# Kernel optimization log

Hardware: AMD Instinct MI355X
Metric: run time of the kernel (lower is better)

The kernel has to match this reference:

```python
import jax, jax.numpy as jnp
import numpy as np
from jax import lax

# config constants (match init_kwargs)
SEQ_LEN = 512
PRED_LEN = 96
ENC_IN = 64
D_MODEL = 128
E_LAYERS = 2
GRAPH_SCALE = 16
GRAPH_RANK = 8
TCN_KERNEL = 3
TCN_DILATION = 2
BATCH = 16


def setup_inputs() -> dict:
    key = jax.random.key(0)
    ks = jax.random.split(key, 12)
    s = 0.02
    inp = {
        "x_enc": jax.random.normal(ks[0], (BATCH, SEQ_LEN, ENC_IN), jnp.float32),
        "x_mark_enc": jnp.zeros((BATCH, SEQ_LEN, 4), jnp.float32),
        "x_dec": jnp.zeros((BATCH, PRED_LEN, ENC_IN), jnp.float32),
        "x_mark_dec": jnp.zeros((BATCH, PRED_LEN, 4), jnp.float32),
        # value embedding (scalar -> d_model)
        "w_emb": jax.random.normal(ks[1], (1, D_MODEL), jnp.float32) * s,
        "b_emb": jnp.zeros((D_MODEL,), jnp.float32),
        # stacked dilated causal conv layers [L, K, Cin, Cout]
        "conv_w": jax.random.normal(ks[2], (E_LAYERS, TCN_KERNEL, D_MODEL, D_MODEL), jnp.float32) * s,
        "conv_b": jnp.zeros((E_LAYERS, D_MODEL), jnp.float32),
        # low-rank graph generator projections
        "gg_w1": jax.random.normal(ks[3], (D_MODEL, GRAPH_RANK), jnp.float32) * s,
        "gg_b1": jnp.zeros((GRAPH_RANK,), jnp.float32),
        "gg_w2": jax.random.normal(ks[4], (D_MODEL, GRAPH_RANK), jnp.float32) * s,
        "gg_b2": jnp.zeros((GRAPH_RANK,), jnp.float32),
        # head: Linear(d_model * num_tokens, pred_len)
        "head_w": jax.random.normal(ks[5], (D_MODEL * SEQ_LEN, PRED_LEN), jnp.float32) * s,
        "head_b": jnp.zeros((PRED_LEN,), jnp.float32),
    }
    return inp


def _tcn(x_enc, w_emb, b_emb, conv_w, conv_b):
    # x_enc: [B, L, N] -> channel-independent per-variable encoding -> [B, N, L, D]
    B, L, N = x_enc.shape
    h = x_enc.transpose(0, 2, 1).reshape(B * N, L, 1) @ w_emb + b_emb  # [B*N, L, D]
    for i in range(conv_w.shape[0]):
        dil = TCN_DILATION ** i
        pad = (TCN_KERNEL - 1) * dil
        hp = jnp.pad(h, ((0, 0), (pad, 0), (0, 0)))  # causal left pad
        y = lax.conv_general_dilated(
            hp, conv_w[i], window_strides=(1,), padding="VALID",
            rhs_dilation=(dil,), dimension_numbers=("NWC", "WIO", "NWC"),
        ) + conv_b[i]
        h = jax.nn.gelu(y) + h  # residual
    return h.reshape(B, N, L, -1)


def _forward(x_enc, w_emb, b_emb, conv_w, conv_b, gg_w1, gg_b1, gg_w2, gg_b2, head_w, head_b):
    h_time = _tcn(x_enc, w_emb, b_emb, conv_w, conv_b)  # [B, N, L, D]
    B, N, L, D = h_time.shape
    S = L // GRAPH_SCALE  # number of segments (L divisible by scale)
    h_seg = h_time.reshape(B, N, S, GRAPH_SCALE, D)
    z = h_seg.mean(axis=3)  # [B, N, S, D] segment summaries
    # low-rank graph generation for all segments at once
    e1 = z @ gg_w1 + gg_b1  # [B, N, S, r]
    e2 = z @ gg_w2 + gg_b2
    scores = jnp.einsum("bnsr,bmsr->bsnm", e1, e2) / jnp.asarray(np.sqrt(GRAPH_RANK), z.dtype)
    adj = jax.nn.softmax(scores, axis=-1)  # [B, S, N, N] row-stochastic
    # adjacency temporal-smoothness regularizer: sum_s mean|adj_s - adj_{s-1}|
    reg = jnp.sum(jnp.mean(jnp.abs(adj[:, 1:] - adj[:, :-1]), axis=(0, 2, 3)))
    # graph-weighted feature mixing per segment
    h_mix = jnp.einsum("bsnm,bmscd->bnscd", adj, h_seg).reshape(B, N, L, D)
    # head over flattened (token, dim)
    out = h_mix.reshape(B, N, L * D) @ head_w + head_b  # [B, N, pred_len]
    return out.transpose(0, 2, 1), reg  # [B, pred_len, N]


def reference(x_enc, x_mark_enc, x_dec, x_mark_dec, w_emb, b_emb, conv_w, conv_b,
              gg_w1, gg_b1, gg_w2, gg_b2, head_w, head_b):
    # x_mark_enc / x_dec / x_mark_dec are unused by forecast path (faithful to source)
    return _forward(x_enc, w_emb, b_emb, conv_w, conv_b, gg_w1, gg_b1, gg_w2, gg_b2, head_w, head_b)
```

## Files before the change

kernel.cpp:

```cpp
#include <hip/hip_runtime.h>
#include <hip/hip_bf16.h>


#define BATCH 16
#define SEQ 512
#define NVAR 64
#define DM 128
#define SEG 32
#define SCL 16
#define RNK 8
#define PRED 96
#define BN (BATCH * NVAR)
#define ROWLEN (SEQ * DM)

typedef unsigned short ushort_t;
typedef __attribute__((ext_vector_type(8))) short short8;
typedef __attribute__((ext_vector_type(4))) float f32x4;

__device__ inline float bf2f(ushort_t u) {
    union { unsigned int i; float f; } x;
    x.i = ((unsigned int)u) << 16;
    return x.f;
}
__device__ inline ushort_t f2bf(float f) {
    union { float f; unsigned int i; } u;
    u.f = f;
    unsigned int x = u.i;
    return (ushort_t)((x + 0x7fffu + ((x >> 16) & 1u)) >> 16);
}
__device__ inline unsigned int pkbf(float a, float b) {
    __hip_bfloat162 h = __float22bfloat162_rn(make_float2(a, b));
    union { __hip_bfloat162 h2; unsigned int u; } c;
    c.h2 = h;
    return c.u;
}
__device__ inline float blo(unsigned int u) {
    union { unsigned int i; float f; } x;
    x.i = u << 16;
    return x.f;
}
__device__ inline float bhi(unsigned int u) {
    union { unsigned int i; float f; } x;
    x.i = u & 0xFFFF0000u;
    return x.f;
}
__device__ inline float gelu_fast(float x) {
    float t = 0.7978845608028654f * x * (1.0f + 0.044715f * x * x);
    float e = __expf(-2.0f * t);
    return x * __builtin_amdgcn_rcpf(1.0f + e);
}

__global__ __launch_bounds__(128) void wt_prep(
    const float* __restrict__ conv_w, const float* __restrict__ w_emb,
    const float* __restrict__ b_emb, const float* __restrict__ conv_b,
    ushort_t* __restrict__ WTf, float* __restrict__ Acoef,
    float* __restrict__ Bias3, float* __restrict__ regacc) {
    if (blockIdx.x == 0 && blockIdx.y == 0 && threadIdx.x == 0) regacc[0] = 0.f;
    if (blockIdx.x < 3) {
        int tap = blockIdx.x;
        int ci = blockIdx.y;
        int co = threadIdx.x;
        int kt = ci >> 5, quad = (ci >> 3) & 3, j = ci & 7;
        int ng = co >> 4, col = co & 15;
        int lane = quad * 16 + col;
        WTf[((((size_t)tap * 4 + kt) * 8 + ng) * 64 + lane) * 8 + j] =
            f2bf(conv_w[(size_t)(3 + tap) * 16384 + (size_t)ci * 128 + co]);
    } else if (blockIdx.y == 0) {
        int co = threadIdx.x;
        float a0 = 0.f, a1 = 0.f, a2 = 0.f, c0 = 0.f, c1 = 0.f, c2 = 0.f;
        for (int ci = 0; ci < 128; ++ci) {
            float we = w_emb[ci], be = b_emb[ci];
            float w0 = conv_w[((size_t)(0 * 128 + ci)) * 128 + co];
            float w1 = conv_w[((size_t)(1 * 128 + ci)) * 128 + co];
            float w2 = conv_w[((size_t)(2 * 128 + ci)) * 128 + co];
            a0 += we * w0; c0 += be * w0;
            a1 += we * w1; c1 += be * w1;
            a2 += we * w2; c2 += be * w2;
        }
        Acoef[0 * 128 + co] = a0;
        Acoef[1 * 128 + co] = a1;
        Acoef[2 * 128 + co] = a2;
        float b0 = conv_b[co];
        Bias3[0 * 128 + co] = b0 + c2;
        Bias3[1 * 128 + co] = b0 + c1 + c2;
        Bias3[2 * 128 + co] = b0 + c0 + c1 + c2;
    }
}

__global__ __launch_bounds__(256, 4) void tcn_mfma(
    const float* __restrict__ x, const float* __restrict__ w_emb,
    const float* __restrict__ b_emb, const float* __restrict__ Acoef,
    const float* __restrict__ Bias3, const ushort_t* __restrict__ WTf,
    const float* __restrict__ conv_b,
    const float* __restrict__ gw1, const float* __restrict__ gb1,
    const float* __restrict__ gw2, const float* __restrict__ gb2,
    ushort_t* __restrict__ h2, float* __restrict__ e1, float* __restrict__ e2) {
    __shared__ __align__(16) ushort_t h1s[68 * 136];
    __shared__ float xs[70];
    __shared__ float zbuf[4 * 128];

    int bn = blockIdx.x;
    int b = bn >> 6, n = bn & 63;
    int chunk = blockIdx.y;
    int l0 = chunk * 64;
    int tid = threadIdx.x;

    {
        const float* xb = x + (size_t)b * SEQ * NVAR + n;
        if (tid < 70) {
            int l = l0 - 6 + tid;
            xs[tid] = (l >= 0) ? xb[(size_t)l * NVAR] : 0.0f;
        }
    }
    __syncthreads();

    {
        int dp = (tid & 63) * 2;
        float2 A0 = *reinterpret_cast<const float2*>(&Acoef[0 * 128 + dp]);
        float2 A1 = *reinterpret_cast<const float2*>(&Acoef[1 * 128 + dp]);
        float2 A2 = *reinterpret_cast<const float2*>(&Acoef[2 * 128 + dp]);
        float2 BF = *reinterpret_cast<const float2*>(&Bias3[2 * 128 + dp]);
        float2 we2 = *reinterpret_cast<const float2*>(&w_emb[dp]);
        float2 be2 = *reinterpret_cast<const float2*>(&b_emb[dp]);
#pragma unroll
        for (int i = 0; i < 17; ++i) {
            int row = (tid >> 6) + 4 * i;
            int l = l0 - 4 + row;
            unsigned int pk = 0;
            if (l >= 0) {
                float x0 = xs[row], x1 = xs[row + 1], x2 = xs[row + 2];
                float2 bias = BF;
                if (l < 2)
                    bias = *reinterpret_cast<const float2*>(&Bias3[l * 128 + dp]);
                float y0 = fmaf(x0, A0.x, fmaf(x1, A1.x, fmaf(x2, A2.x, bias.x)));
                float y1 = fmaf(x0, A0.y, fmaf(x1, A1.y, fmaf(x2, A2.y, bias.y)));
                float r0 = gelu_fast(y0) + fmaf(x2, we2.x, be2.x);
                float r1 = gelu_fast(y1) + fmaf(x2, we2.y, be2.y);
                pk = pkbf(r0, r1);
            }
            *reinterpret_cast<unsigned int*>(&h1s[row * 136 + dp]) = pk;
        }
    }
    __syncthreads();

    int lane = tid & 63;
    int wv = tid >> 6;
    int quad = lane >> 4;
    int col = lane & 15;
    int cobase = wv * 32;

    f32x4 acc2[4][2];
#pragma unroll
    for (int mt = 0; mt < 4; ++mt)
#pragma unroll
        for (int nt = 0; nt < 2; ++nt)
            acc2[mt][nt] = (f32x4){0.f, 0.f, 0.f, 0.f};

#pragma unroll
    for (int tap = 0; tap < 3; ++tap) {
        short8 wf0[4], wf1[4];
#pragma unroll
        for (int kt = 0; kt < 4; ++kt) {
            const ushort_t* bp =
                WTf + ((((size_t)tap * 4 + kt) * 8 + wv * 2) * 64 + lane) * 8;
            wf0[kt] = *(const short8*)bp;
            wf1[kt] = *(const short8*)(bp + 512);
        }
#pragma unroll
        for (int kt = 0; kt < 4; ++kt) {
            int kc = kt * 32 + quad * 8;
#pragma unroll
            for (int mt = 0; mt < 4; ++mt) {
                short8 hf = *(const short8*)&h1s[(mt * 16 + col + 2 * tap) * 136 + kc];
                acc2[mt][0] = __builtin_amdgcn_mfma_f32_16x16x32_bf16(wf0[kt], hf, acc2[mt][0], 0, 0, 0);
                acc2[mt][1] = __builtin_amdgcn_mfma_f32_16x16x32_bf16(wf1[kt], hf, acc2[mt][1], 0, 0, 0);
            }
        }
    }

    {
        uint2 res[4][2];
#pragma unroll
        for (int mt = 0; mt < 4; ++mt) {
            int li = mt * 16 + col;
#pragma unroll
            for (int nt = 0; nt < 2; ++nt) {
                int co = cobase + nt * 16 + quad * 4;
                res[mt][nt] = *reinterpret_cast<const uint2*>(
                    &h1s[(li + 4) * 136 + co]);
            }
        }
        __syncthreads();
        float4 bias[2];
        bias[0] = *reinterpret_cast<const float4*>(&conv_b[DM + cobase + quad * 4]);
        bias[1] = *reinterpret_cast<const float4*>(&conv_b[DM + cobase + 16 + quad * 4]);
#pragma unroll
        for (int mt = 0; mt < 4; ++mt) {
            int li = mt * 16 + col;
#pragma unroll
            for (int nt = 0; nt < 2; ++nt) {
                int co = cobase + nt * 16 + quad * 4;
                float h0 = gelu_fast(acc2[mt][nt][0] + bias[nt].x) + blo(res[mt][nt].x);
                float h1 = gelu_fast(acc2[mt][nt][1] + bias[nt].y) + bhi(res[mt][nt].x);
                float h2v = gelu_fast(acc2[mt][nt][2] + bias[nt].z) + blo(res[mt][nt].y);
                float h3 = gelu_fast(acc2[mt][nt][3] + bias[nt].w) + bhi(res[mt][nt].y);
                uint2 pk;
                pk.x = pkbf(h0, h1);
                pk.y = pkbf(h2v, h3);
                *reinterpret_cast<uint2*>(&h1s[li * 136 + co]) = pk;
            }
        }
    }
    __syncthreads();

    {
        ushort_t* orow = h2 + (size_t)bn * ROWLEN + (size_t)l0 * 128;
#pragma unroll
        for (int i = 0; i < 4; ++i) {
            int q = tid + 256 * i;
            int row = q >> 4, c8 = (q & 15) * 8;
            *(short8*)&orow[row * 128 + c8] = *(const short8*)&h1s[row * 136 + c8];
        }
    }
    {
        int d = tid & 127, sg = tid >> 7;
#pragma unroll
        for (int t = 0; t < 2; ++t) {
            int sl = sg + 2 * t;
            float a = 0.0f;
#pragma unroll
            for (int c = 0; c < SCL; ++c)
                a += bf2f(h1s[(sl * 16 + c) * 136 + d]);
            zbuf[sl * 128 + d] = a * (1.0f / 16.0f);
        }
    }
    __syncthreads();
    {
        int out = tid >> 2;
        int part = tid & 3;
        int sl = out >> 4;
        int which = (out >> 3) & 1;
        int r = out & 7;
        const float* w = which ? gw2 : gw1;
        float a = 0.0f;
        int d0 = part * 32;
        for (int d = d0; d < d0 + 32; ++d)
            a += zbuf[sl * 128 + d] * w[d * RNK + r];
        a += __shfl_xor(a, 1, 64);
        a += __shfl_xor(a, 2, 64);
        if (part == 0) {
            a += (which ? gb2 : gb1)[r];
            int s = chunk * 4 + sl;
            (which ? e2 : e1)[(((size_t)b * SEG + s) * NVAR + n) * RNK + r] = a;
        }
    }
}

__global__ __launch_bounds__(256) void g_gemm(
    const ushort_t* __restrict__ h2, const float* __restrict__ head_w,
    float* __restrict__ G) {
    __shared__ __align__(16) ushort_t As[64 * 72];
    __shared__ __align__(16) ushort_t Bs[96 * 72];
    int s = blockIdx.x;
    int bnt = blockIdx.y;
    int kh = blockIdx.z;
    int bn0 = bnt * 64;
    int kbase = kh * 1024;
    int lane = threadIdx.x & 63, wv = threadIdx.x >> 6;
    int quad = lane >> 4, col = lane & 15;
    int mh = wv & 1;
    int ph = wv >> 1;

    int arow = threadIdx.x >> 2, akq = (threadIdx.x & 3) * 16;
    const ushort_t* aptr =
        h2 + (size_t)(bn0 + arow) * ROWLEN + (size_t)s * 2048 + kbase + akq;
    const float* bbase = head_w + ((size_t)s * 2048 + kbase) * PRED;
    int bp0[3], bk2[3];
#pragma unroll
    for (int i = 0; i < 3; ++i) {
        int q = threadIdx.x + 256 * i;
        bp0[i] = (q % 24) * 4;
        bk2[i] = (q / 24) * 2;
    }

    f32x4 acc[3][2];
#pragma unroll
    for (int i = 0; i < 3; ++i)
#pragma unroll
        for (int j = 0; j < 2; ++j) acc[i][j] = (f32x4){0.f, 0.f, 0.f, 0.f};

    short8 pa0 = *(const short8*)aptr;
    short8 pa1 = *(const short8*)(aptr + 8);
    float4 pb0[3], pb1[3];
#pragma unroll
    for (int i = 0; i < 3; ++i) {
        const float* src = bbase + (size_t)bk2[i] * PRED + bp0[i];
        pb0[i] = *reinterpret_cast<const float4*>(src);
        pb1[i] = *reinterpret_cast<const float4*>(src + PRED);
    }
    *(short8*)&As[arow * 72 + akq] = pa0;
    *(short8*)&As[arow * 72 + akq + 8] = pa1;
#pragma unroll
    for (int i = 0; i < 3; ++i) {
        *reinterpret_cast<unsigned int*>(&Bs[(bp0[i] + 0) * 72 + bk2[i]]) = pkbf(pb0[i].x, pb1[i].x);
        *reinterpret_cast<unsigned int*>(&Bs[(bp0[i] + 1) * 72 + bk2[i]]) = pkbf(pb0[i].y, pb1[i].y);
        *reinterpret_cast<unsigned int*>(&Bs[(bp0[i] + 2) * 72 + bk2[i]]) = pkbf(pb0[i].z, pb1[i].z);
        *reinterpret_cast<unsigned int*>(&Bs[(bp0[i] + 3) * 72 + bk2[i]]) = pkbf(pb0[i].w, pb1[i].w);
    }
    __syncthreads();

    for (int kt = 0; kt < 16; ++kt) {
        if (kt < 15) {
            const ushort_t* ap = aptr + (kt + 1) * 64;
            pa0 = *(const short8*)ap;
            pa1 = *(const short8*)(ap + 8);
#pragma unroll
            for (int i = 0; i < 3; ++i) {
                const float* src =
                    bbase + (size_t)((kt + 1) * 64 + bk2[i]) * PRED + bp0[i];
                pb0[i] = *reinterpret_cast<const float4*>(src);
                pb1[i] = *reinterpret_cast<const float4*>(src + PRED);
            }
        }
#pragma unroll
        for (int kk = 0; kk < 2; ++kk) {
            int kc = kk * 32 + quad * 8;
            short8 pfr[3];
#pragma unroll
            for (int i = 0; i < 3; ++i)
                pfr[i] = *(const short8*)&Bs[(ph * 48 + i * 16 + col) * 72 + kc];
#pragma unroll
            for (int j = 0; j < 2; ++j) {
                short8 bnfr = *(const short8*)&As[(mh * 32 + j * 16 + col) * 72 + kc];
#pragma unroll
                for (int i = 0; i < 3; ++i)
                    acc[i][j] = __builtin_amdgcn_mfma_f32_16x16x32_bf16(pfr[i], bnfr, acc[i][j], 0, 0, 0);
            }
        }
        __syncthreads();
        if (kt < 15) {
            *(short8*)&As[arow * 72 + akq] = pa0;
            *(short8*)&As[arow * 72 + akq + 8] = pa1;
#pragma unroll
            for (int i = 0; i < 3; ++i) {
                *reinterpret_cast<unsigned int*>(&Bs[(bp0[i] + 0) * 72 + bk2[i]]) = pkbf(pb0[i].x, pb1[i].x);
                *reinterpret_cast<unsigned int*>(&Bs[(bp0[i] + 1) * 72 + bk2[i]]) = pkbf(pb0[i].y, pb1[i].y);
                *reinterpret_cast<unsigned int*>(&Bs[(bp0[i] + 2) * 72 + bk2[i]]) = pkbf(pb0[i].z, pb1[i].z);
                *reinterpret_cast<unsigned int*>(&Bs[(bp0[i] + 3) * 72 + bk2[i]]) = pkbf(pb0[i].w, pb1[i].w);
            }
            __syncthreads();
        }
    }
    int b = bnt;
#pragma unroll
    for (int i = 0; i < 3; ++i)
#pragma unroll
        for (int j = 0; j < 2; ++j)
#pragma unroll
            for (int r = 0; r < 4; ++r) {
                int p = ph * 48 + i * 16 + quad * 4 + r;
                int m = mh * 32 + j * 16 + col;
                atomicAdd(&G[(((size_t)s * BATCH + b) * PRED + p) * NVAR + m],
                          acc[i][j][r]);
            }
}

__global__ __launch_bounds__(256) void out_partial(
    const float* __restrict__ e1, const float* __restrict__ e2,
    const float* __restrict__ G, float* __restrict__ partial,
    float* __restrict__ regacc) {
    __shared__ float adjn[2][32][65];
    __shared__ float Gs[96][65];
    __shared__ float e2s[3][64][8];
    __shared__ float e1s[3][32][8];
    __shared__ float wsum[4];
    int b = blockIdx.x, sg = blockIdx.y, nh = blockIdx.z;
    int s0 = sg * 2;
    int wv = threadIdx.x >> 6, lane = threadIdx.x & 63;

    for (int idx = threadIdx.x; idx < 3 * 64 * 8; idx += 256) {
        int j = idx >> 9, m = (idx >> 3) & 63, r = idx & 7;
        int s = s0 - 1 + j;
        e2s[j][m][r] = (s >= 0)
            ? e2[(((size_t)b * SEG + s) * NVAR + m) * RNK + r] : 0.0f;
    }
    for (int idx = threadIdx.x; idx < 3 * 32 * 8; idx += 256) {
        int j = idx >> 8, nl = (idx >> 3) & 31, r = idx & 7;
        int s = s0 - 1 + j;
        e1s[j][nl][r] = (s >= 0)
            ? e1[(((size_t)b * SEG + s) * NVAR + nh * 32 + nl) * RNK + r] : 0.0f;
    }
    __syncthreads();

    float regsum = 0.0f;
    for (int t = 0; t < 8; ++t) {
        int nl = wv * 8 + t;
        float a[3];
#pragma unroll
        for (int j = 0; j < 3; ++j) {
            float sc = 0.0f;
#pragma unroll
            for (int r = 0; r < 8; ++r) sc += e1s[j][nl][r] * e2s[j][lane][r];
            sc *= 0.35355339059327373f;
            float mx = sc;
            for (int off = 32; off; off >>= 1)
                mx = fmaxf(mx, __shfl_xor(mx, off, 64));
            float ex = __expf(sc - mx);
            float sm = ex;
            for (int off = 32; off; off >>= 1) sm += __shfl_xor(sm, off, 64);
            a[j] = ex * __builtin_amdgcn_rcpf(sm);
        }
        if (s0 > 0) regsum += fabsf(a[1] - a[0]);
        regsum += fabsf(a[2] - a[1]);
        adjn[0][nl][lane] = a[1];
        adjn[1][nl][lane] = a[2];
    }
    __syncthreads();

    int pg = threadIdx.x >> 4;
    int ng = threadIdx.x & 15;
    float acc[6][2];
#pragma unroll
    for (int j = 0; j < 6; ++j) { acc[j][0] = 0.f; acc[j][1] = 0.f; }

#pragma unroll
    for (int ss = 0; ss < 2; ++ss) {
        int s = s0 + ss;
#pragma unroll
        for (int i = 0; i < 6; ++i) {
            int q = threadIdx.x + 256 * i;
            int row = q >> 4, mq = (q & 15) * 4;
            float4 v = *reinterpret_cast<const float4*>(
                &G[(((size_t)s * BATCH + b) * PRED + row) * NVAR + mq]);
            Gs[row][mq + 0] = v.x; Gs[row][mq + 1] = v.y;
            Gs[row][mq + 2] = v.z; Gs[row][mq + 3] = v.w;
        }
        __syncthreads();
#pragma unroll 4
        for (int m = 0; m < 64; ++m) {
            float a0 = adjn[ss][ng * 2 + 0][m];
            float a1 = adjn[ss][ng * 2 + 1][m];
#pragma unroll
            for (int j = 0; j < 6; ++j) {
                float g = Gs[pg * 6 + j][m];
                acc[j][0] += g * a0;
                acc[j][1] += g * a1;
            }
        }
        __syncthreads();
    }
#pragma unroll
    for (int j = 0; j < 6; ++j)
#pragma unroll
        for (int i = 0; i < 2; ++i) {
            int p = pg * 6 + j, n = nh * 32 + ng * 2 + i;
            partial[(((size_t)sg * BATCH + b) * PRED + p) * NVAR + n] = acc[j][i];
        }
    for (int off = 32; off; off >>= 1) regsum += __shfl_xor(regsum, off, 64);
    if (lane == 0) wsum[wv] = regsum;
    __syncthreads();
    if (threadIdx.x == 0)
        atomicAdd(regacc, wsum[0] + wsum[1] + wsum[2] + wsum[3]);
}

__global__ __launch_bounds__(256) void out_reduce(
    const float* __restrict__ partial, const float* __restrict__ head_b,
    const float* __restrict__ regacc, float* __restrict__ out, int out_size) {
    int i4 = blockIdx.x * 256 + threadIdx.x;
    int p = (i4 >> 4) % PRED;
    float hb = head_b[p];
    float4 a = make_float4(hb, hb, hb, hb);
    const int stride4 = BATCH * PRED * NVAR / 4;
    const float4* p4 = reinterpret_cast<const float4*>(partial);
#pragma unroll
    for (int sg = 0; sg < 16; ++sg) {
        float4 v = p4[sg * stride4 + i4];
        a.x += v.x; a.y += v.y; a.z += v.z; a.w += v.w;
    }
    reinterpret_cast<float4*>(out)[i4] = a;
    if (i4 == 0) out[out_size - 1] = regacc[0] * (1.0f / 65536.0f);
}

extern "C" void kernel_launch(void* const* d_in, const int* in_sizes, int n_in,
                              void* d_out, int out_size, void* d_ws,
                              size_t ws_size, hipStream_t stream) {
    const float* x_enc  = (const float*)d_in[0];
    const float* w_emb  = (const float*)d_in[4];
    const float* b_emb  = (const float*)d_in[5];
    const float* conv_w = (const float*)d_in[6];
    const float* conv_b = (const float*)d_in[7];
    const float* gg_w1  = (const float*)d_in[8];
    const float* gg_b1  = (const float*)d_in[9];
    const float* gg_w2  = (const float*)d_in[10];
    const float* gg_b2  = (const float*)d_in[11];
    const float* head_w = (const float*)d_in[12];
    const float* head_b = (const float*)d_in[13];
    float* out = (float*)d_out;

    char* ws = (char*)d_ws;
    ushort_t* h2   = (ushort_t*)(ws);
    float* partial = (float*)(ws);
    float* G       = (float*)(ws + 134217728);
    float* e1      = (float*)(ws + 146800640);
    float* e2      = (float*)(ws + 147849216);
    ushort_t* WTf  = (ushort_t*)(ws + 148897792);
    float* Acoef   = (float*)(ws + 148996096);
    float* Bias3   = (float*)(ws + 148997632);
    float* regacc  = (float*)(ws + 157286400);

    hipMemsetAsync(G, 0, 12582912, stream);
    wt_prep<<<dim3(4, 128), 128, 0, stream>>>(
        conv_w, w_emb, b_emb, conv_b, WTf, Acoef, Bias3, regacc);
    tcn_mfma<<<dim3(BN, SEQ / 64), 256, 0, stream>>>(
        x_enc, w_emb, b_emb, Acoef, Bias3, WTf, conv_b,
        gg_w1, gg_b1, gg_w2, gg_b2, h2, e1, e2);
    g_gemm<<<dim3(SEG, BATCH, 2), 256, 0, stream>>>(h2, head_w, G);
    out_partial<<<dim3(BATCH, 16, 2), 256, 0, stream>>>(
        e1, e2, G, partial, regacc);
    out_reduce<<<BATCH * PRED * NVAR / 1024, 256, 0, stream>>>(
        partial, head_b, regacc, out, out_size);
}
```

Before: 312.5 us.

## Pre-pack head weights to bf16 fragment layout and drop atomics in head GEMM

Adds an hw_prep kernel that converts head_w from fp32 into a bf16 layout matching the MFMA fragment order. g_gemm then loads B fragments straight from global memory into registers, with double buffering, instead of staging and converting them through shared memory every tile. The two K halves become two sequential launches that store and then accumulate into G, which removes the atomics and the memset. The cost is two extra prep launches, an extra bf16 copy of head_w in memory, and a serial split of the K halves. GELU is also rewritten with a folded constant and a raw v_exp_f32 instruction.

```diff
diff --git a/kernel.cpp b/kernel.cpp
--- a/kernel.cpp
+++ b/kernel.cpp
@@ -45,8 +45,10 @@
     return x.f;
 }
 __device__ inline float gelu_fast(float x) {
-    float t = 0.7978845608028654f * x * (1.0f + 0.044715f * x * x);
-    float e = __expf(-2.0f * t);
+    float x2 = x * x;
+    float t2 = x * fmaf(-0.10294854f, x2, -2.3022584f);
+    float e;
+    asm("v_exp_f32 %0, %1" : "=v"(e) : "v"(t2));
     return x * __builtin_amdgcn_rcpf(1.0f + e);
 }
 
@@ -87,6 +89,26 @@
     }
 }
 
+__global__ __launch_bounds__(256) void hw_prep(
+    const float* __restrict__ head_w, ushort_t* __restrict__ HWf, int kh) {
+    __shared__ float ts[32 * 97];
+    int k32p = blockIdx.x;
+    int s = k32p >> 5, t = k32p & 31;
+    int kbase = (s * 64 + kh * 32 + t) * 32;
+    const float* src = head_w + (size_t)kbase * 96;
+    for (int idx = threadIdx.x; idx < 3072; idx += 256) {
+        int kk = idx / 96, p = idx - kk * 96;
+        ts[kk * 97 + p] = src[idx];
+    }
+    __syncthreads();
+    unsigned int* ob32 =
+        reinterpret_cast<unsigned int*>(HWf + (size_t)k32p * 3072);
+    for (int odx = threadIdx.x; odx < 1536; odx += 256) {
+        int p = odx >> 4, kk = (odx & 15) * 2;
+        ob32[odx] = pkbf(ts[kk * 97 + p], ts[(kk + 1) * 97 + p]);
+    }
+}
+
 __global__ __launch_bounds__(256, 4) void tcn_mfma(
     const float* __restrict__ x, const float* __restrict__ w_emb,
     const float* __restrict__ b_emb, const float* __restrict__ Acoef,
@@ -257,31 +279,24 @@
 }
 
 __global__ __launch_bounds__(256) void g_gemm(
-    const ushort_t* __restrict__ h2, const float* __restrict__ head_w,
-    float* __restrict__ G) {
-    __shared__ __align__(16) ushort_t As[64 * 72];
-    __shared__ __align__(16) ushort_t Bs[96 * 72];
+    const ushort_t* __restrict__ h2, const ushort_t* __restrict__ HWf,
+    float* __restrict__ G, int kh, int first) {
+    __shared__ __align__(16) ushort_t As[2][64 * 72];
     int s = blockIdx.x;
     int bnt = blockIdx.y;
-    int kh = blockIdx.z;
     int bn0 = bnt * 64;
     int kbase = kh * 1024;
     int lane = threadIdx.x & 63, wv = threadIdx.x >> 6;
     int quad = lane >> 4, col = lane & 15;
     int mh = wv & 1;
     int ph = wv >> 1;
+    int p0 = ph * 48 + col;
 
     int arow = threadIdx.x >> 2, akq = (threadIdx.x & 3) * 16;
     const ushort_t* aptr =
         h2 + (size_t)(bn0 + arow) * ROWLEN + (size_t)s * 2048 + kbase + akq;
-    const float* bbase = head_w + ((size_t)s * 2048 + kbase) * PRED;
-    int bp0[3], bk2[3];
-#pragma unroll
-    for (int i = 0; i < 3; ++i) {
-        int q = threadIdx.x + 256 * i;
-        bp0[i] = (q % 24) * 4;
-        bk2[i] = (q / 24) * 2;
-    }
+    const ushort_t* hb =
+        HWf + (size_t)s * 98304 + (size_t)p0 * 32 + quad * 8;
 
     f32x4 acc[3][2];
 #pragma unroll
@@ -291,67 +306,51 @@
 
     short8 pa0 = *(const short8*)aptr;
     short8 pa1 = *(const short8*)(aptr + 8);
-    float4 pb0[3], pb1[3];
-#pragma unroll
-    for (int i = 0; i < 3; ++i) {
-        const float* src = bbase + (size_t)bk2[i] * PRED + bp0[i];
-        pb0[i] = *reinterpret_cast<const float4*>(src);
-        pb1[i] = *reinterpret_cast<const float4*>(src + PRED);
-    }
-    *(short8*)&As[arow * 72 + akq] = pa0;
-    *(short8*)&As[arow * 72 + akq + 8] = pa1;
-#pragma unroll
-    for (int i = 0; i < 3; ++i) {
-        *reinterpret_cast<unsigned int*>(&Bs[(bp0[i] + 0) * 72 + bk2[i]]) = pkbf(pb0[i].x, pb1[i].x);
-        *reinterpret_cast<unsigned int*>(&Bs[(bp0[i] + 1) * 72 + bk2[i]]) = pkbf(pb0[i].y, pb1[i].y);
-        *reinterpret_cast<unsigned int*>(&Bs[(bp0[i] + 2) * 72 + bk2[i]]) = pkbf(pb0[i].z, pb1[i].z);
-        *reinterpret_cast<unsigned int*>(&Bs[(bp0[i] + 3) * 72 + bk2[i]]) = pkbf(pb0[i].w, pb1[i].w);
-    }
-    __syncthreads();
-
+    short8 pf[2][2][3];
+#pragma unroll
+    for (int kk = 0; kk < 2; ++kk)
+#pragma unroll
+        for (int i = 0; i < 3; ++i)
+            pf[0][kk][i] = *(const short8*)(hb + kk * 3072 + i * 512);
+    *(short8*)&As[0][arow * 72 + akq] = pa0;
+    *(short8*)&As[0][arow * 72 + akq + 8] = pa1;
+    __syncthreads();
+
+#pragma unroll
     for (int kt = 0; kt < 16; ++kt) {
+        const int par = kt & 1;
         if (kt < 15) {
             const ushort_t* ap = aptr + (kt + 1) * 64;
             pa0 = *(const short8*)ap;
             pa1 = *(const short8*)(ap + 8);
-#pragma unroll
-            for (int i = 0; i < 3; ++i) {
-                const float* src =
-                    bbase + (size_t)((kt + 1) * 64 + bk2[i]) * PRED + bp0[i];
-                pb0[i] = *reinterpret_cast<const float4*>(src);
-                pb1[i] = *reinterpret_cast<const float4*>(src + PRED);
-            }
+            const ushort_t* fb = hb + (size_t)(kt + 1) * 6144;
+#pragma unroll
+            for (int kk = 0; kk < 2; ++kk)
+#pragma unroll
+                for (int i = 0; i < 3; ++i)
+                    pf[par ^ 1][kk][i] =
+                        *(const short8*)(fb + kk * 3072 + i * 512);
         }
 #pragma unroll
         for (int kk = 0; kk < 2; ++kk) {
             int kc = kk * 32 + quad * 8;
-            short8 pfr[3];
-#pragma unroll
-            for (int i = 0; i < 3; ++i)
-                pfr[i] = *(const short8*)&Bs[(ph * 48 + i * 16 + col) * 72 + kc];
 #pragma unroll
             for (int j = 0; j < 2; ++j) {
-                short8 bnfr = *(const short8*)&As[(mh * 32 + j * 16 + col) * 72 + kc];
+                short8 bnfr =
+                    *(const short8*)&As[par][(mh * 32 + j * 16 + col) * 72 + kc];
 #pragma unroll
                 for (int i = 0; i < 3; ++i)
-                    acc[i][j] = __builtin_amdgcn_mfma_f32_16x16x32_bf16(pfr[i], bnfr, acc[i][j], 0, 0, 0);
-            }
+                    acc[i][j] = __builtin_amdgcn_mfma_f32_16x16x32_bf16(
+                        pf[par][kk][i], bnfr, acc[i][j], 0, 0, 0);
+            }
+        }
+        if (kt < 15) {
+            *(short8*)&As[par ^ 1][arow * 72 + akq] = pa0;
+            *(short8*)&As[par ^ 1][arow * 72 + akq + 8] = pa1;
         }
         __syncthreads();
-        if (kt < 15) {
-            *(short8*)&As[arow * 72 + akq] = pa0;
-            *(short8*)&As[arow * 72 + akq + 8] = pa1;
-#pragma unroll
-            for (int i = 0; i < 3; ++i) {
-                *reinterpret_cast<unsigned int*>(&Bs[(bp0[i] + 0) * 72 + bk2[i]]) = pkbf(pb0[i].x, pb1[i].x);
-                *reinterpret_cast<unsigned int*>(&Bs[(bp0[i] + 1) * 72 + bk2[i]]) = pkbf(pb0[i].y, pb1[i].y);
-                *reinterpret_cast<unsigned int*>(&Bs[(bp0[i] + 2) * 72 + bk2[i]]) = pkbf(pb0[i].z, pb1[i].z);
-                *reinterpret_cast<unsigned int*>(&Bs[(bp0[i] + 3) * 72 + bk2[i]]) = pkbf(pb0[i].w, pb1[i].w);
-            }
-            __syncthreads();
-        }
-    }
-    int b = bnt;
+    }
+
 #pragma unroll
     for (int i = 0; i < 3; ++i)
 #pragma unroll
@@ -360,8 +359,9 @@
             for (int r = 0; r < 4; ++r) {
                 int p = ph * 48 + i * 16 + quad * 4 + r;
                 int m = mh * 32 + j * 16 + col;
-                atomicAdd(&G[(((size_t)s * BATCH + b) * PRED + p) * NVAR + m],
-                          acc[i][j][r]);
+                size_t o = (((size_t)s * BATCH + bnt) * PRED + p) * NVAR + m;
+                if (first) G[o] = acc[i][j][r];
+                else G[o] += acc[i][j][r];
             }
 }
 
@@ -506,15 +506,18 @@
     ushort_t* WTf  = (ushort_t*)(ws + 148897792);
     float* Acoef   = (float*)(ws + 148996096);
     float* Bias3   = (float*)(ws + 148997632);
+    ushort_t* HWf  = (ushort_t*)(ws + 149000192);
     float* regacc  = (float*)(ws + 157286400);
 
-    hipMemsetAsync(G, 0, 12582912, stream);
     wt_prep<<<dim3(4, 128), 128, 0, stream>>>(
         conv_w, w_emb, b_emb, conv_b, WTf, Acoef, Bias3, regacc);
     tcn_mfma<<<dim3(BN, SEQ / 64), 256, 0, stream>>>(
         x_enc, w_emb, b_emb, Acoef, Bias3, WTf, conv_b,
         gg_w1, gg_b1, gg_w2, gg_b2, h2, e1, e2);
-    g_gemm<<<dim3(SEG, BATCH, 2), 256, 0, stream>>>(h2, head_w, G);
+    hw_prep<<<1024, 256, 0, stream>>>(head_w, HWf, 0);
+    g_gemm<<<dim3(SEG, BATCH), 256, 0, stream>>>(h2, HWf, G, 0, 1);
+    hw_prep<<<1024, 256, 0, stream>>>(head_w, HWf, 1);
+    g_gemm<<<dim3(SEG, BATCH), 256, 0, stream>>>(h2, HWf, G, 1, 0);
     out_partial<<<dim3(BATCH, 16, 2), 256, 0, stream>>>(
         e1, e2, G, partial, regacc);
     out_reduce<<<BATCH * PRED * NVAR / 1024, 256, 0, stream>>>(
```

Measured after the change: 297.1 us. 1.05x faster.
